# Performance work log

Measured on AMD Instinct MI355X. Metric: run time of the kernel, lower is better.

## Reference

```python
import jax, jax.numpy as jnp
import numpy as np

D = 2048      # hidden
H = 16        # heads
HD = 128      # head dim
E = 64        # experts
K = 8         # top-k
F = 1024      # expert intermediate
B, S = 1, 256
EPS = 1e-05
THETA = 10000.0
SCALE = 0.08838834764831845  # 1/sqrt(128)


def _rms(x, w):
    return x * jax.lax.rsqrt(jnp.mean(x * x, axis=-1, keepdims=True) + EPS) * w


def _rotate_half(x):
    h = x.shape[-1] // 2
    return jnp.concatenate([-x[..., h:], x[..., :h]], axis=-1)


def setup_inputs() -> dict:
    key = jax.random.key(0)
    ks = jax.random.split(key, 16)
    std = 0.02
    return {
        "x": jax.random.normal(ks[0], (B, S, D), jnp.float32),
        "ln1_w": jnp.ones((D,), jnp.float32),
        "q_w": jax.random.normal(ks[1], (D, D), jnp.float32) * std,
        "k_w": jax.random.normal(ks[2], (D, D), jnp.float32) * std,
        "v_w": jax.random.normal(ks[3], (D, D), jnp.float32) * std,
        "o_w": jax.random.normal(ks[4], (D, D), jnp.float32) * std,
        "qn_w": jnp.ones((D,), jnp.float32),
        "kn_w": jnp.ones((D,), jnp.float32),
        "ln2_w": jnp.ones((D,), jnp.float32),
        "router_w": jax.random.normal(ks[5], (E, D), jnp.float32) * std,
        "gate_w": jax.random.normal(ks[6], (E, F, D), jnp.float32) * std,
        "up_w": jax.random.normal(ks[7], (E, F, D), jnp.float32) * std,
        "down_w": jax.random.normal(ks[8], (E, D, F), jnp.float32) * std,
    }


def reference(x, ln1_w, q_w, k_w, v_w, o_w, qn_w, kn_w, ln2_w,
              router_w, gate_w, up_w, down_w):
    b, s, d = x.shape
    # ---- attention ----
    xn = _rms(x, ln1_w)
    q = _rms(jnp.einsum('bsd,od->bso', xn, q_w), qn_w)
    k = _rms(jnp.einsum('bsd,od->bso', xn, k_w), kn_w)
    v = jnp.einsum('bsd,od->bso', xn, v_w)
    q = q.reshape(b, s, H, HD).transpose(0, 2, 1, 3)  # [b,h,s,hd]
    k = k.reshape(b, s, H, HD).transpose(0, 2, 1, 3)
    v = v.reshape(b, s, H, HD).transpose(0, 2, 1, 3)
    # RoPE
    inv_freq = 1.0 / (THETA ** (jnp.arange(0, HD, 2, dtype=jnp.float32) / HD))
    ang = jnp.arange(s, dtype=jnp.float32)[:, None] * inv_freq[None, :]  # [s, hd/2]
    emb = jnp.concatenate([ang, ang], axis=-1)
    cos, sin = jnp.cos(emb).astype(x.dtype), jnp.sin(emb).astype(x.dtype)
    q = q * cos + _rotate_half(q) * sin
    k = k * cos + _rotate_half(k) * sin
    scores = jnp.einsum('bhqd,bhkd->bhqk', q, k) * SCALE
    causal = jnp.tril(jnp.ones((s, s), bool))
    scores = jnp.where(causal, scores, jnp.finfo(scores.dtype).min)
    attn = jax.nn.softmax(scores, axis=-1)
    ctx = jnp.einsum('bhqk,bhkd->bhqd', attn, v)
    ctx = ctx.transpose(0, 2, 1, 3).reshape(b, s, d)
    h = x + jnp.einsum('bsd,od->bso', ctx, o_w)
    # ---- MoE ----
    hn = _rms(h, ln2_w)
    logits = jnp.einsum('bsd,ed->bse', hn, router_w)
    probs = jax.nn.softmax(logits.astype(jnp.float32), axis=-1)
    vals, idx = jax.lax.top_k(probs, K)  # [b,s,K]
    # dense combine weights [b,s,E]; OLMoE does not renormalize top-k probs
    combine = jnp.sum(jax.nn.one_hot(idx, E, dtype=jnp.float32) * vals[..., None], axis=-2)
    combine = combine.reshape(-1, E).astype(x.dtype)  # [T,E]
    xf = hn.reshape(-1, d)                            # [T,D]
    g = jnp.einsum('td,efd->etf', xf, gate_w)         # [E,T,F]
    u = jnp.einsum('td,efd->etf', xf, up_w)
    mid = jax.nn.silu(g) * u
    eo = jnp.einsum('etf,edf->etd', mid, down_w)      # [E,T,D]
    y = jnp.einsum('te,etd->td', combine, eo).reshape(b, s, d)
    return h + y
```

## Files before the change

### kernel.cpp

```cpp
#include <hip/hip_runtime.h>
#include <math.h>

#define DHID 2048
#define TOK 256
#define NHEAD 16
#define HDIM 128
#define NEXP 64
#define KSEL 8
#define FFD 1024
#define RMSEPS 1e-5f
#define ATTNSCALE 0.08838834764831845f

typedef short bf16x8 __attribute__((ext_vector_type(8)));
typedef float f32x4 __attribute__((ext_vector_type(4)));

__device__ __forceinline__ unsigned short f2bf(float f){
  union { float f; unsigned int u; } c; c.f = f;
  unsigned int u = c.u + 0x7fffu + ((c.u>>16)&1u);
  return (unsigned short)(u>>16);
}
__device__ __forceinline__ unsigned int pk2(float a, float b){
  return (unsigned int)f2bf(a) | ((unsigned int)f2bf(b)<<16);
}
__device__ __forceinline__ bf16x8 as_bf8(uint4 u){
  union { uint4 u; bf16x8 v; } c; c.u = u; return c.v;
}

#define WAITV(N) { asm volatile("s_waitcnt vmcnt(" #N ")" ::: "memory"); __builtin_amdgcn_sched_barrier(0); }
#define WAITL0   { asm volatile("s_waitcnt lgkmcnt(0)" ::: "memory"); __builtin_amdgcn_sched_barrier(0); }
#define SB       __builtin_amdgcn_sched_barrier(0);

__global__ __launch_bounds__(256) void rms_kernel(const float* __restrict__ x,
    const float* __restrict__ w, unsigned short* __restrict__ obf,
    float* __restrict__ of32)
{
  int row = blockIdx.x, tid = threadIdx.x;
  const float* xr = x + (size_t)row*DHID;
  float4 a = *(const float4*)(xr + tid*8);
  float4 b = *(const float4*)(xr + tid*8 + 4);
  float ss = a.x*a.x+a.y*a.y+a.z*a.z+a.w*a.w + b.x*b.x+b.y*b.y+b.z*b.z+b.w*b.w;
  #pragma unroll
  for(int o=32;o>0;o>>=1) ss += __shfl_down(ss,o);
  __shared__ float red[4];
  if((tid&63)==0) red[tid>>6]=ss;
  __syncthreads();
  float r = rsqrtf((red[0]+red[1]+red[2]+red[3])*(1.0f/DHID) + RMSEPS);
  float v[8] = {a.x,a.y,a.z,a.w,b.x,b.y,b.z,b.w};
  unsigned short ob[8];
  #pragma unroll
  for(int j=0;j<8;j++){
    float val = v[j]*r*w[tid*8+j];
    ob[j]=f2bf(val);
    if(of32) of32[(size_t)row*DHID + tid*8 + j] = val;
  }
  uint4 o4;
  o4.x = (unsigned int)ob[0] | ((unsigned int)ob[1]<<16);
  o4.y = (unsigned int)ob[2] | ((unsigned int)ob[3]<<16);
  o4.z = (unsigned int)ob[4] | ((unsigned int)ob[5]<<16);
  o4.w = (unsigned int)ob[6] | ((unsigned int)ob[7]<<16);
  *(uint4*)(obf + (size_t)row*DHID + tid*8) = o4;
}

__global__ void rope_table_kernel(float* __restrict__ cs, float* __restrict__ sn){
  int i = blockIdx.x*256 + threadIdx.x;
  int s = i>>6, j = i&63;
  float invf = powf(10000.0f, -(float)j*(1.0f/64.0f));
  float ang = (float)s * invf;
  cs[i] = cosf(ang); sn[i] = sinf(ang);
}

__global__ __launch_bounds__(256) void gemm_qkv_kernel(
    const unsigned short* __restrict__ A,
    const float* __restrict__ qw, const float* __restrict__ kw, const float* __restrict__ vw,
    float* __restrict__ qo, float* __restrict__ ko, float* __restrict__ vo)
{
  int nt = blockIdx.x, mt = blockIdx.y;
  int which = nt>>5, nb = nt&31;
  const float* W = (which==0)? qw : (which==1)? kw : vw;
  float* OUT = (which==0)? qo : (which==1)? ko : vo;
  int n0 = nb*64, m0 = mt*64;
  __shared__ unsigned short As[64*64];
  __shared__ unsigned short Bs[64*64];
  int tid = threadIdx.x;
  int wid = tid>>6, lane = tid&63;
  int wm = wid>>1, wn = wid&1;
  int lr = lane&15, lg = lane>>4;
  int sr = tid>>2, sq = tid&3;
  f32x4 acc[2][2] = {};
  const unsigned short* Ap = A + (size_t)(m0+sr)*DHID + sq*16;
  const float* Bp = W + (size_t)(n0+sr)*DHID + sq*16;
  for(int k0=0;k0<DHID;k0+=64){
    uint4 a0 = *(const uint4*)(Ap + k0);
    uint4 a1 = *(const uint4*)(Ap + k0 + 8);
    float4 b0 = *(const float4*)(Bp + k0);
    float4 b1 = *(const float4*)(Bp + k0 + 4);
    float4 b2 = *(const float4*)(Bp + k0 + 8);
    float4 b3 = *(const float4*)(Bp + k0 + 12);
    int x7 = sr&7;
    *(uint4*)&As[sr*64 + (((sq*2)  ^ x7)*8)] = a0;
    *(uint4*)&As[sr*64 + (((sq*2+1)^ x7)*8)] = a1;
    uint4 p0 = make_uint4(pk2(b0.x,b0.y),pk2(b0.z,b0.w),pk2(b1.x,b1.y),pk2(b1.z,b1.w));
    uint4 p1 = make_uint4(pk2(b2.x,b2.y),pk2(b2.z,b2.w),pk2(b3.x,b3.y),pk2(b3.z,b3.w));
    *(uint4*)&Bs[sr*64 + (((sq*2)  ^ x7)*8)] = p0;
    *(uint4*)&Bs[sr*64 + (((sq*2+1)^ x7)*8)] = p1;
    __syncthreads();
    #pragma unroll
    for(int ki=0;ki<2;ki++){
      bf16x8 af[2], bfr[2];
      #pragma unroll
      for(int mi=0;mi<2;mi++){
        int r = wm*32 + mi*16 + lr;
        af[mi] = *(const bf16x8*)&As[r*64 + (((ki*4+lg)^(r&7))*8)];
      }
      #pragma unroll
      for(int ni=0;ni<2;ni++){
        int r = wn*32 + ni*16 + lr;
        bfr[ni] = *(const bf16x8*)&Bs[r*64 + (((ki*4+lg)^(r&7))*8)];
      }
      #pragma unroll
      for(int mi=0;mi<2;mi++)
        #pragma unroll
        for(int ni=0;ni<2;ni++)
          acc[mi][ni] = __builtin_amdgcn_mfma_f32_16x16x32_bf16(af[mi], bfr[ni], acc[mi][ni], 0,0,0);
    }
    __syncthreads();
  }
  #pragma unroll
  for(int mi=0;mi<2;mi++){
    #pragma unroll
    for(int ni=0;ni<2;ni++){
      int col = n0 + wn*32 + ni*16 + lr;
      int rowb = m0 + wm*32 + mi*16 + lg*4;
      #pragma unroll
      for(int rg=0;rg<4;rg++)
        OUT[(size_t)(rowb+rg)*DHID + col] = acc[mi][ni][rg];
    }
  }
}

__global__ __launch_bounds__(256) void gemm_o_kernel(const float* __restrict__ A,
  const float* __restrict__ W, const float* __restrict__ X,
  float* __restrict__ H, float* __restrict__ O)
{
  int nb = blockIdx.x, mt = blockIdx.y;
  int n0 = nb*64, m0 = mt*64;
  __shared__ unsigned short As[64*64];
  __shared__ unsigned short Bs[64*64];
  int tid = threadIdx.x;
  int wid = tid>>6, lane = tid&63;
  int wm = wid>>1, wn = wid&1;
  int lr = lane&15, lg = lane>>4;
  int sr = tid>>2, sq = tid&3;
  f32x4 acc[2][2] = {};
  const float* Ap = A + (size_t)(m0+sr)*DHID + sq*16;
  const float* Bp = W + (size_t)(n0+sr)*DHID + sq*16;
  for(int k0=0;k0<DHID;k0+=64){
    float4 a0=*(const float4*)(Ap+k0),   a1=*(const float4*)(Ap+k0+4);
    float4 a2=*(const float4*)(Ap+k0+8), a3=*(const float4*)(Ap+k0+12);
    float4 b0=*(const float4*)(Bp+k0),   b1=*(const float4*)(Bp+k0+4);
    float4 b2=*(const float4*)(Bp+k0+8), b3=*(const float4*)(Bp+k0+12);
    int x7 = sr&7;
    uint4 pa0 = make_uint4(pk2(a0.x,a0.y),pk2(a0.z,a0.w),pk2(a1.x,a1.y),pk2(a1.z,a1.w));
    uint4 pa1 = make_uint4(pk2(a2.x,a2.y),pk2(a2.z,a2.w),pk2(a3.x,a3.y),pk2(a3.z,a3.w));
    uint4 pb0 = make_uint4(pk2(b0.x,b0.y),pk2(b0.z,b0.w),pk2(b1.x,b1.y),pk2(b1.z,b1.w));
    uint4 pb1 = make_uint4(pk2(b2.x,b2.y),pk2(b2.z,b2.w),pk2(b3.x,b3.y),pk2(b3.z,b3.w));
    *(uint4*)&As[sr*64 + (((sq*2)  ^ x7)*8)] = pa0;
    *(uint4*)&As[sr*64 + (((sq*2+1)^ x7)*8)] = pa1;
    *(uint4*)&Bs[sr*64 + (((sq*2)  ^ x7)*8)] = pb0;
    *(uint4*)&Bs[sr*64 + (((sq*2+1)^ x7)*8)] = pb1;
    __syncthreads();
    #pragma unroll
    for(int ki=0;ki<2;ki++){
      bf16x8 af[2], bfr[2];
      #pragma unroll
      for(int mi=0;mi<2;mi++){
        int r = wm*32 + mi*16 + lr;
        af[mi] = *(const bf16x8*)&As[r*64 + (((ki*4+lg)^(r&7))*8)];
      }
      #pragma unroll
      for(int ni=0;ni<2;ni++){
        int r = wn*32 + ni*16 + lr;
        bfr[ni] = *(const bf16x8*)&Bs[r*64 + (((ki*4+lg)^(r&7))*8)];
      }
      #pragma unroll
      for(int mi=0;mi<2;mi++)
        #pragma unroll
        for(int ni=0;ni<2;ni++)
          acc[mi][ni] = __builtin_amdgcn_mfma_f32_16x16x32_bf16(af[mi], bfr[ni], acc[mi][ni], 0,0,0);
    }
    __syncthreads();
  }
  #pragma unroll
  for(int mi=0;mi<2;mi++){
    #pragma unroll
    for(int ni=0;ni<2;ni++){
      int col = n0 + wn*32 + ni*16 + lr;
      int rowb = m0 + wm*32 + mi*16 + lg*4;
      #pragma unroll
      for(int rg=0;rg<4;rg++){
        size_t idx = (size_t)(rowb+rg)*DHID + col;
        float v = acc[mi][ni][rg] + X[idx];
        H[idx] = v; O[idx] = v;
      }
    }
  }
}

__global__ __launch_bounds__(256) void qknorm_rope_kernel(const float* __restrict__ in,
   const float* __restrict__ w, const float* __restrict__ cs, const float* __restrict__ sn,
   float* __restrict__ out)
{
  int t = blockIdx.x, tid = threadIdx.x;
  __shared__ float xs[DHID];
  const float* xr = in + (size_t)t*DHID;
  float4 a = *(const float4*)(xr + tid*8);
  float4 b = *(const float4*)(xr + tid*8 + 4);
  *(float4*)&xs[tid*8] = a; *(float4*)&xs[tid*8+4] = b;
  float ss = a.x*a.x+a.y*a.y+a.z*a.z+a.w*a.w + b.x*b.x+b.y*b.y+b.z*b.z+b.w*b.w;
  #pragma unroll
  for(int o=32;o>0;o>>=1) ss += __shfl_down(ss,o);
  __shared__ float red[4];
  if((tid&63)==0) red[tid>>6]=ss;
  __syncthreads();
  float r = rsqrtf((red[0]+red[1]+red[2]+red[3])*(1.0f/DHID) + RMSEPS);
  int hh = tid>>4, jb = (tid&15)*4;
  #pragma unroll
  for(int p=0;p<4;p++){
    int j = jb+p;
    int i0 = hh*HDIM + j, i1 = i0+64;
    float va = xs[i0]*r*w[i0];
    float vb = xs[i1]*r*w[i1];
    float c = cs[t*64+j], s = sn[t*64+j];
    out[((size_t)(hh*TOK + t))*HDIM + j]    = va*c - vb*s;
    out[((size_t)(hh*TOK + t))*HDIM + j+64] = vb*c + va*s;
  }
}

__global__ __launch_bounds__(256) void attn_kernel(const float* __restrict__ qh,
  const float* __restrict__ kh, const float* __restrict__ vf, float* __restrict__ ctx)
{
  int head = blockIdx.x>>4, qt = blockIdx.x&15;
  __shared__ float qs[16][132];
  __shared__ float sc[16][260];
  __shared__ float red[16][16];
  __shared__ float rmx[16], rsm[16];
  int tid = threadIdx.x;
  {
    int r = tid>>4, c = (tid&15)*8;
    const float* src = qh + ((size_t)(head*TOK + qt*16 + r))*HDIM + c;
    *(float4*)&qs[r][c]   = *(const float4*)(src);
    *(float4*)&qs[r][c+4] = *(const float4*)(src+4);
  }
  __syncthreads();
  int qi = tid&15, kk = tid>>4;
  int qg = qt*16 + qi;
  for(int k=kk; k<=qg; k+=16){
    const float* kp = kh + ((size_t)(head*TOK + k))*HDIM;
    float d = 0.f;
    #pragma unroll 8
    for(int c=0;c<128;c+=4){
      float4 kv = *(const float4*)(kp + c);
      float4 qv = *(const float4*)&qs[qi][c];
      d += qv.x*kv.x + qv.y*kv.y + qv.z*kv.z + qv.w*kv.w;
    }
    sc[qi][k] = d*ATTNSCALE;
  }
  float m = -1e30f;
  for(int k=kk;k<=qg;k+=16) m = fmaxf(m, sc[qi][k]);
  red[qi][kk] = m;
  __syncthreads();
  if(kk==0){
    float mm=-1e30f;
    #pragma unroll
    for(int j=0;j<16;j++) mm = fmaxf(mm, red[qi][j]);
    rmx[qi]=mm;
  }
  __syncthreads();
  float mm = rmx[qi];
  float s = 0.f;
  for(int k=kk;k<=qg;k+=16){ float pp = expf(sc[qi][k]-mm); sc[qi][k]=pp; s+=pp; }
  red[qi][kk]=s;
  __syncthreads();
  if(kk==0){
    float t_=0.f;
    #pragma unroll
    for(int j=0;j<16;j++) t_ += red[qi][j];
    rsm[qi]=t_;
  }
  __syncthreads();
  int dg = kk;
  float acc[8]={0,0,0,0,0,0,0,0};
  const float* vp = vf + head*HDIM + dg*8;
  for(int k=0;k<=qg;k++){
    float p = sc[qi][k];
    float4 v0 = *(const float4*)(vp + (size_t)k*DHID);
    float4 v1 = *(const float4*)(vp + (size_t)k*DHID + 4);
    acc[0]+=p*v0.x; acc[1]+=p*v0.y; acc[2]+=p*v0.z; acc[3]+=p*v0.w;
    acc[4]+=p*v1.x; acc[5]+=p*v1.y; acc[6]+=p*v1.z; acc[7]+=p*v1.w;
  }
  float inv = 1.0f/rsm[qi];
  float* op = ctx + ((size_t)(qt*16+qi))*DHID + head*HDIM + dg*8;
  *(float4*)(op)   = make_float4(acc[0]*inv, acc[1]*inv, acc[2]*inv, acc[3]*inv);
  *(float4*)(op+4) = make_float4(acc[4]*inv, acc[5]*inv, acc[6]*inv, acc[7]*inv);
}

__global__ __launch_bounds__(256) void router_kernel(const float* __restrict__ hn,
    const float* __restrict__ rw, int* __restrict__ counts, int* __restrict__ toklist,
    float* __restrict__ wlist)
{
  int t = blockIdx.x, tid = threadIdx.x;
  __shared__ float xs[DHID];
  __shared__ float part[NEXP*4];
  __shared__ float probs[NEXP];
  *(float4*)&xs[tid*8]   = *(const float4*)(hn + (size_t)t*DHID + tid*8);
  *(float4*)&xs[tid*8+4] = *(const float4*)(hn + (size_t)t*DHID + tid*8+4);
  __syncthreads();
  int e = tid&63, c = tid>>6;
  const float* w = rw + (size_t)e*DHID + c*512;
  const float* xc = xs + c*512;
  float d = 0.f;
  for(int i=0;i<512;i+=4){
    float4 wv = *(const float4*)(w+i);
    d += xc[i]*wv.x + xc[i+1]*wv.y + xc[i+2]*wv.z + xc[i+3]*wv.w;
  }
  part[c*64 + e] = d;
  __syncthreads();
  if(tid<64){
    float logit = part[tid] + part[64+tid] + part[128+tid] + part[192+tid];
    float m = logit;
    #pragma unroll
    for(int o=32;o>0;o>>=1) m = fmaxf(m, __shfl_xor(m,o));
    float p = expf(logit - m);
    float s = p;
    #pragma unroll
    for(int o=32;o>0;o>>=1) s += __shfl_xor(s,o);
    probs[tid] = p/s;
  }
  __syncthreads();
  if(tid==0){
    unsigned long long used = 0ull;
    for(int r=0;r<KSEL;r++){
      float best = -1.f; int bi = 0;
      for(int j=0;j<NEXP;j++){
        if(!((used>>j)&1ull) && probs[j]>best){ best=probs[j]; bi=j; }
      }
      used |= (1ull<<bi);
      int slot = atomicAdd(&counts[bi],1);
      toklist[bi*TOK+slot] = t;
      wlist[bi*TOK+slot] = best;
    }
  }
}

__global__ void scan_kernel(const int* __restrict__ counts, int* __restrict__ offs){
  int e = threadIdx.x;
  int c = counts[e];
  int v = c;
  #pragma unroll
  for(int o=1;o<64;o<<=1){
    int n = __shfl_up(v,o);
    if(e>=o) v += n;
  }
  offs[e] = v - c;
}

__global__ __launch_bounds__(256,2) void moe_gateup_kernel(const unsigned short* __restrict__ hnb,
  const float* __restrict__ gw, const float* __restrict__ uw,
  const int* __restrict__ counts, const int* __restrict__ offs,
  const int* __restrict__ toklist, const float* __restrict__ wlist,
  unsigned short* __restrict__ mid)
{
  int fb = blockIdx.x, e = blockIdx.y, mc = blockIdx.z;
  int cnt = counts[e];
  if(mc*32 >= cnt) return;
  int base = offs[e];
  __shared__ unsigned short Gs[64*256];
  __shared__ unsigned short Us[64*256];
  int tid = threadIdx.x, w = tid>>6, lane = tid&63;
  int wm = w>>1, wn = w&1, lr = lane&15, lg = lane>>4;
  int srow = tid>>2, sc4 = tid&3, rx = srow&7;
  int halfo = (sc4&1)*4, vbase = sc4>>1;

  const float* Gp = gw + ((size_t)e*FFD + fb*64 + srow)*DHID + sc4*4;
  const float* Up = uw + ((size_t)e*FFD + fb*64 + srow)*DHID + sc4*4;
  int aslot = mc*32 + wm*16 + lr;
  int acl = (aslot<cnt)? aslot : (cnt-1);
  const unsigned short* Ap = hnb + (size_t)toklist[e*TOK+acl]*DHID + lg*8;

  f32x4 ag[2]={}, au[2]={};
  float4 P[8], Q[8];
  uint4 av[8];

  #define ISSUE(BK,SRC,s,jb) { \
    _Pragma("unroll") \
    for(int j=0;j<8;j++) BK[j] = *(const float4*)(SRC + (s)*256 + ((jb)+j)*16); }
  #define WRITE(BK,DST,jb) { \
    _Pragma("unroll") \
    for(int j=0;j<8;j++){ \
      int v = ((jb)+j)*2 + vbase; \
      int vp = (v & ~7) | ((v&7) ^ rx); \
      uint2 val; val.x = pk2(BK[j].x,BK[j].y); val.y = pk2(BK[j].z,BK[j].w); \
      *(uint2*)&DST[srow*256 + vp*8 + halfo] = val; } }
  #define ISSUE_A(s) { \
    _Pragma("unroll") \
    for(int kf=0;kf<8;kf++) av[kf] = *(const uint4*)(Ap + (s)*256 + kf*32); }
  #define COMPUTE() { \
    _Pragma("unroll") \
    for(int kf=0;kf<8;kf++){ \
      bf16x8 af = as_bf8(av[kf]); \
      _Pragma("unroll") \
      for(int ni=0;ni<2;ni++){ \
        int R = wn*32 + ni*16 + lr; \
        int v = kf*4 + lg; \
        int vp = (v & ~7) | ((v&7) ^ (lr&7)); \
        int ho = R*256 + vp*8; \
        bf16x8 gfr = *(const bf16x8*)&Gs[ho]; \
        bf16x8 ufr = *(const bf16x8*)&Us[ho]; \
        ag[ni] = __builtin_amdgcn_mfma_f32_16x16x32_bf16(af, gfr, ag[ni], 0,0,0); \
        au[ni] = __builtin_amdgcn_mfma_f32_16x16x32_bf16(af, ufr, au[ni], 0,0,0); \
      } \
    } }

  const int NS = DHID/256;
  ISSUE(P, Gp, 0, 0)
  ISSUE(Q, Gp, 0, 8)
  for(int s=0;s<NS;s++){
    WAITV(8)
    WRITE(P, Gs, 0)
    ISSUE(P, Up, s, 0)
    WAITV(8)
    WRITE(Q, Gs, 8)
    ISSUE(Q, Up, s, 8)
    WAITV(8)
    WRITE(P, Us, 0)
    ISSUE_A(s)
    WAITV(8)
    WRITE(Q, Us, 8)
    if(s+1<NS){ ISSUE(P, Gp, s+1, 0) }
    WAITL0
    __builtin_amdgcn_s_barrier(); SB
    if(s+1<NS){ WAITV(8) } else { WAITV(0) }
    COMPUTE()
    if(s+1<NS){ ISSUE(Q, Gp, s+1, 8) }
    __builtin_amdgcn_s_barrier(); SB
  }
  #undef ISSUE
  #undef WRITE
  #undef ISSUE_A
  #undef COMPUTE

  #pragma unroll
  for(int ni=0;ni<2;ni++){
    int f = fb*64 + wn*32 + ni*16 + lr;
    #pragma unroll
    for(int rg=0;rg<4;rg++){
      int sl = wm*16 + lg*4 + rg;
      int slot = mc*32 + sl;
      if(slot < cnt){
        float cw = wlist[e*TOK + slot];
        float g = ag[ni][rg], u = au[ni][rg];
        float mval = g/(1.0f+expf(-g))*u*cw;
        mid[((size_t)(base+slot))*FFD + f] = f2bf(mval);
      }
    }
  }
}

__global__ __launch_bounds__(256,3) void moe_down_kernel(const unsigned short* __restrict__ mid,
  const float* __restrict__ dwn, const int* __restrict__ counts, const int* __restrict__ offs,
  const int* __restrict__ toklist, float* __restrict__ out)
{
  int nb=blockIdx.x, e=blockIdx.y, mc=blockIdx.z;
  int cnt=counts[e];
  if(mc*32>=cnt) return;
  int base=offs[e];
  __shared__ unsigned short Ds[64*256];
  int tid=threadIdx.x, w=tid>>6, lane=tid&63;
  int wm=w>>1, wn=w&1, lr=lane&15, lg=lane>>4;
  int srow=tid>>2, sc4=tid&3, rx=srow&7;
  int halfo=(sc4&1)*4, vbase=sc4>>1;

  const float* Dp = dwn + ((size_t)e*DHID + nb*64 + srow)*FFD + sc4*4;
  int slot0 = mc*32 + wm*16 + lr;
  int sla = (slot0<cnt)? slot0 : (cnt-1);
  const unsigned short* Ap = mid + (size_t)(base+sla)*FFD + lg*8;

  f32x4 acc[2]={};
  float4 P[8], Q[8];
  uint4 av[8];

  #define ISSUE(BK,s,jb) { \
    _Pragma("unroll") \
    for(int j=0;j<8;j++) BK[j] = *(const float4*)(Dp + (s)*256 + ((jb)+j)*16); }
  #define WRITE(BK,jb) { \
    _Pragma("unroll") \
    for(int j=0;j<8;j++){ \
      int v = ((jb)+j)*2 + vbase; \
      int vp = (v & ~7) | ((v&7) ^ rx); \
      uint2 val; val.x = pk2(BK[j].x,BK[j].y); val.y = pk2(BK[j].z,BK[j].w); \
      *(uint2*)&Ds[srow*256 + vp*8 + halfo] = val; } }
  #define ISSUE_A(s) { \
    _Pragma("unroll") \
    for(int kf=0;kf<8;kf++) av[kf] = *(const uint4*)(Ap + (s)*256 + kf*32); }
  #define COMPUTE() { \
    _Pragma("unroll") \
    for(int kf=0;kf<8;kf++){ \
      bf16x8 af = as_bf8(av[kf]); \
      _Pragma("unroll") \
      for(int ni=0;ni<2;ni++){ \
        int R = wn*32 + ni*16 + lr; \
        int v = kf*4 + lg; \
        int vp = (v & ~7) | ((v&7) ^ (lr&7)); \
        bf16x8 dfr = *(const bf16x8*)&Ds[R*256 + vp*8]; \
        acc[ni] = __builtin_amdgcn_mfma_f32_16x16x32_bf16(af, dfr, acc[ni], 0,0,0); \
      } \
    } }

  const int NS = FFD/256;
  ISSUE(P, 0, 0)
  ISSUE(Q, 0, 8)
  for(int s=0;s<NS;s++){
    WAITV(8)
    WRITE(P, 0)
    ISSUE_A(s)
    WAITV(8)
    WRITE(Q, 8)
    if(s+1<NS){ ISSUE(P, s+1, 0) }
    WAITL0
    __builtin_amdgcn_s_barrier(); SB
    if(s+1<NS){ WAITV(8) } else { WAITV(0) }
    COMPUTE()
    if(s+1<NS){ ISSUE(Q, s+1, 8) }
    __builtin_amdgcn_s_barrier(); SB
  }
  #undef ISSUE
  #undef WRITE
  #undef ISSUE_A
  #undef COMPUTE

  #pragma unroll
  for(int ni=0;ni<2;ni++){
    int d = nb*64 + wn*32 + ni*16 + lr;
    #pragma unroll
    for(int rg=0;rg<4;rg++){
      int sl=wm*16+lg*4+rg, slot=mc*32+sl;
      if(slot<cnt){
        int tok = toklist[e*TOK + slot];
        atomicAdd(out + (size_t)tok*DHID + d, acc[ni][rg]);
      }
    }
  }
}

extern "C" void kernel_launch(void* const* d_in, const int* in_sizes, int n_in,
                              void* d_out, int out_size, void* d_ws, size_t ws_size,
                              hipStream_t stream)
{
  (void)in_sizes; (void)n_in; (void)out_size; (void)ws_size;
  const float* x    = (const float*)d_in[0];
  const float* ln1w = (const float*)d_in[1];
  const float* qw   = (const float*)d_in[2];
  const float* kw   = (const float*)d_in[3];
  const float* vw   = (const float*)d_in[4];
  const float* ow   = (const float*)d_in[5];
  const float* qnw  = (const float*)d_in[6];
  const float* knw  = (const float*)d_in[7];
  const float* ln2w = (const float*)d_in[8];
  const float* rw   = (const float*)d_in[9];
  const float* gw   = (const float*)d_in[10];
  const float* uw   = (const float*)d_in[11];
  const float* dwn  = (const float*)d_in[12];
  float* out = (float*)d_out;

  char* p = (char*)d_ws;
  auto alloc = [&](size_t bytes)->void*{ void* r = (void*)p; p += (bytes + 255) & ~(size_t)255; return r; };
  unsigned short* xnb = (unsigned short*)alloc((size_t)TOK*DHID*2);
  float* qf   = (float*)alloc((size_t)TOK*DHID*4);
  float* kf   = (float*)alloc((size_t)TOK*DHID*4);
  float* vf   = (float*)alloc((size_t)TOK*DHID*4);
  float* qh   = (float*)alloc((size_t)TOK*DHID*4);
  float* kh   = (float*)alloc((size_t)TOK*DHID*4);
  float* ctx  = (float*)alloc((size_t)TOK*DHID*4);
  float* hbuf = (float*)alloc((size_t)TOK*DHID*4);
  float* hnf  = (float*)alloc((size_t)TOK*DHID*4);
  unsigned short* hnb = (unsigned short*)alloc((size_t)TOK*DHID*2);
  float* csb  = (float*)alloc((size_t)TOK*64*4);
  float* snb  = (float*)alloc((size_t)TOK*64*4);
  int* counts = (int*)alloc(NEXP*4);
  int* offs   = (int*)alloc(NEXP*4);
  int* toklist= (int*)alloc((size_t)NEXP*TOK*4);
  float* wlist= (float*)alloc((size_t)NEXP*TOK*4);
  unsigned short* mid = (unsigned short*)alloc((size_t)TOK*KSEL*FFD*2);

  rope_table_kernel<<<64,256,0,stream>>>(csb,snb);
  rms_kernel<<<TOK,256,0,stream>>>(x, ln1w, xnb, nullptr);
  gemm_qkv_kernel<<<dim3(96,4),256,0,stream>>>(xnb,qw,kw,vw,qf,kf,vf);
  qknorm_rope_kernel<<<TOK,256,0,stream>>>(qf,qnw,csb,snb,qh);
  qknorm_rope_kernel<<<TOK,256,0,stream>>>(kf,knw,csb,snb,kh);
  attn_kernel<<<256,256,0,stream>>>(qh,kh,vf,ctx);
  gemm_o_kernel<<<dim3(32,4),256,0,stream>>>(ctx,ow,x,hbuf,out);
  rms_kernel<<<TOK,256,0,stream>>>(hbuf, ln2w, hnb, hnf);
  hipMemsetAsync(counts,0,NEXP*4,stream);
  router_kernel<<<TOK,256,0,stream>>>(hnf,rw,counts,toklist,wlist);
  scan_kernel<<<1,64,0,stream>>>(counts,offs);
  moe_gateup_kernel<<<dim3(16,NEXP,8),256,0,stream>>>(hnb,gw,uw,counts,offs,toklist,wlist,mid);
  moe_down_kernel<<<dim3(32,NEXP,8),256,0,stream>>>(mid,dwn,counts,offs,toklist,out);
}
```

Before: 642.2 us.

## Drop rope-table and scan launches, compute inline; use nontemporal weight loads

The RoPE cos/sin table kernel is removed and the angles are computed inline with powf/cosf/sinf in the qk-norm kernel. The expert-offset scan kernel is removed; each MoE block recomputes the prefix sum over counts with wave shuffles and shares it through LDS after a barrier. Expert weight loads in the gate/up and down kernels now use nontemporal loads so the streamed fp32 weights are less likely to pollute the cache. This saves two kernel launches but adds redundant transcendental and scan work per block, plus an extra __syncthreads.

New measurement: 691.9 us. +7.7%, slower.

```diff
diff --git a/kernel.cpp b/kernel.cpp
--- a/kernel.cpp
+++ b/kernel.cpp
@@ -13,6 +13,8 @@
 
 typedef short bf16x8 __attribute__((ext_vector_type(8)));
 typedef float f32x4 __attribute__((ext_vector_type(4)));
+typedef float f4 __attribute__((ext_vector_type(4)));
+typedef unsigned int u4 __attribute__((ext_vector_type(4)));
 
 __device__ __forceinline__ unsigned short f2bf(float f){
   union { float f; unsigned int u; } c; c.f = f;
@@ -59,14 +61,6 @@
   o4.z = (unsigned int)ob[4] | ((unsigned int)ob[5]<<16);
   o4.w = (unsigned int)ob[6] | ((unsigned int)ob[7]<<16);
   *(uint4*)(obf + (size_t)row*DHID + tid*8) = o4;
-}
-
-__global__ void rope_table_kernel(float* __restrict__ cs, float* __restrict__ sn){
-  int i = blockIdx.x*256 + threadIdx.x;
-  int s = i>>6, j = i&63;
-  float invf = powf(10000.0f, -(float)j*(1.0f/64.0f));
-  float ang = (float)s * invf;
-  cs[i] = cosf(ang); sn[i] = sinf(ang);
 }
 
 __global__ __launch_bounds__(256) void gemm_qkv_kernel(
@@ -207,8 +201,7 @@
 }
 
 __global__ __launch_bounds__(256) void qknorm_rope_kernel(const float* __restrict__ in,
-   const float* __restrict__ w, const float* __restrict__ cs, const float* __restrict__ sn,
-   float* __restrict__ out)
+   const float* __restrict__ w, float* __restrict__ out)
 {
   int t = blockIdx.x, tid = threadIdx.x;
   __shared__ float xs[DHID];
@@ -230,7 +223,9 @@
     int i0 = hh*HDIM + j, i1 = i0+64;
     float va = xs[i0]*r*w[i0];
     float vb = xs[i1]*r*w[i1];
-    float c = cs[t*64+j], s = sn[t*64+j];
+    float invf = powf(10000.0f, -(float)j*(1.0f/64.0f));
+    float ang = (float)t * invf;
+    float c = cosf(ang), s = sinf(ang);
     out[((size_t)(hh*TOK + t))*HDIM + j]    = va*c - vb*s;
     out[((size_t)(hh*TOK + t))*HDIM + j+64] = vb*c + va*s;
   }
@@ -352,31 +347,27 @@
   }
 }
 
-__global__ void scan_kernel(const int* __restrict__ counts, int* __restrict__ offs){
-  int e = threadIdx.x;
-  int c = counts[e];
-  int v = c;
-  #pragma unroll
-  for(int o=1;o<64;o<<=1){
-    int n = __shfl_up(v,o);
-    if(e>=o) v += n;
-  }
-  offs[e] = v - c;
-}
-
 __global__ __launch_bounds__(256,2) void moe_gateup_kernel(const unsigned short* __restrict__ hnb,
   const float* __restrict__ gw, const float* __restrict__ uw,
-  const int* __restrict__ counts, const int* __restrict__ offs,
+  const int* __restrict__ counts,
   const int* __restrict__ toklist, const float* __restrict__ wlist,
   unsigned short* __restrict__ mid)
 {
   int fb = blockIdx.x, e = blockIdx.y, mc = blockIdx.z;
   int cnt = counts[e];
   if(mc*32 >= cnt) return;
-  int base = offs[e];
+  int tid = threadIdx.x;
+  __shared__ int sbase;
+  if(tid<64){
+    int c = counts[tid];
+    int v = c;
+    #pragma unroll
+    for(int o=1;o<64;o<<=1){ int n=__shfl_up(v,o); if(tid>=o) v+=n; }
+    if(tid==e) sbase = v - c;
+  }
   __shared__ unsigned short Gs[64*256];
   __shared__ unsigned short Us[64*256];
-  int tid = threadIdx.x, w = tid>>6, lane = tid&63;
+  int w = tid>>6, lane = tid&63;
   int wm = w>>1, wn = w&1, lr = lane&15, lg = lane>>4;
   int srow = tid>>2, sc4 = tid&3, rx = srow&7;
   int halfo = (sc4&1)*4, vbase = sc4>>1;
@@ -386,20 +377,22 @@
   int aslot = mc*32 + wm*16 + lr;
   int acl = (aslot<cnt)? aslot : (cnt-1);
   const unsigned short* Ap = hnb + (size_t)toklist[e*TOK+acl]*DHID + lg*8;
+  __syncthreads();
+  int base = sbase;
 
   f32x4 ag[2]={}, au[2]={};
-  float4 P[8], Q[8];
+  f4 P[8], Q[8];
   uint4 av[8];
 
   #define ISSUE(BK,SRC,s,jb) { \
     _Pragma("unroll") \
-    for(int j=0;j<8;j++) BK[j] = *(const float4*)(SRC + (s)*256 + ((jb)+j)*16); }
+    for(int j=0;j<8;j++) BK[j] = __builtin_nontemporal_load((const f4*)(SRC + (s)*256 + ((jb)+j)*16)); }
   #define WRITE(BK,DST,jb) { \
     _Pragma("unroll") \
     for(int j=0;j<8;j++){ \
       int v = ((jb)+j)*2 + vbase; \
       int vp = (v & ~7) | ((v&7) ^ rx); \
-      uint2 val; val.x = pk2(BK[j].x,BK[j].y); val.y = pk2(BK[j].z,BK[j].w); \
+      uint2 val; val.x = pk2(BK[j][0],BK[j][1]); val.y = pk2(BK[j][2],BK[j][3]); \
       *(uint2*)&DST[srow*256 + vp*8 + halfo] = val; } }
   #define ISSUE_A(s) { \
     _Pragma("unroll") \
@@ -467,37 +460,47 @@
 }
 
 __global__ __launch_bounds__(256,3) void moe_down_kernel(const unsigned short* __restrict__ mid,
-  const float* __restrict__ dwn, const int* __restrict__ counts, const int* __restrict__ offs,
+  const float* __restrict__ dwn, const int* __restrict__ counts,
   const int* __restrict__ toklist, float* __restrict__ out)
 {
   int nb=blockIdx.x, e=blockIdx.y, mc=blockIdx.z;
   int cnt=counts[e];
   if(mc*32>=cnt) return;
-  int base=offs[e];
+  int tid=threadIdx.x;
+  __shared__ int sbase;
+  if(tid<64){
+    int c = counts[tid];
+    int v = c;
+    #pragma unroll
+    for(int o=1;o<64;o<<=1){ int n=__shfl_up(v,o); if(tid>=o) v+=n; }
+    if(tid==e) sbase = v - c;
+  }
   __shared__ unsigned short Ds[64*256];
-  int tid=threadIdx.x, w=tid>>6, lane=tid&63;
+  int w=tid>>6, lane=tid&63;
   int wm=w>>1, wn=w&1, lr=lane&15, lg=lane>>4;
   int srow=tid>>2, sc4=tid&3, rx=srow&7;
   int halfo=(sc4&1)*4, vbase=sc4>>1;
 
   const float* Dp = dwn + ((size_t)e*DHID + nb*64 + srow)*FFD + sc4*4;
+  __syncthreads();
+  int base = sbase;
   int slot0 = mc*32 + wm*16 + lr;
   int sla = (slot0<cnt)? slot0 : (cnt-1);
   const unsigned short* Ap = mid + (size_t)(base+sla)*FFD + lg*8;
 
   f32x4 acc[2]={};
-  float4 P[8], Q[8];
+  f4 P[8], Q[8];
   uint4 av[8];
 
   #define ISSUE(BK,s,jb) { \
     _Pragma("unroll") \
-    for(int j=0;j<8;j++) BK[j] = *(const float4*)(Dp + (s)*256 + ((jb)+j)*16); }
+    for(int j=0;j<8;j++) BK[j] = __builtin_nontemporal_load((const f4*)(Dp + (s)*256 + ((jb)+j)*16)); }
   #define WRITE(BK,jb) { \
     _Pragma("unroll") \
     for(int j=0;j<8;j++){ \
       int v = ((jb)+j)*2 + vbase; \
       int vp = (v & ~7) | ((v&7) ^ rx); \
-      uint2 val; val.x = pk2(BK[j].x,BK[j].y); val.y = pk2(BK[j].z,BK[j].w); \
+      uint2 val; val.x = pk2(BK[j][0],BK[j][1]); val.y = pk2(BK[j][2],BK[j][3]); \
       *(uint2*)&Ds[srow*256 + vp*8 + halfo] = val; } }
   #define ISSUE_A(s) { \
     _Pragma("unroll") \
@@ -584,25 +587,20 @@
   float* hbuf = (float*)alloc((size_t)TOK*DHID*4);
   float* hnf  = (float*)alloc((size_t)TOK*DHID*4);
   unsigned short* hnb = (unsigned short*)alloc((size_t)TOK*DHID*2);
-  float* csb  = (float*)alloc((size_t)TOK*64*4);
-  float* snb  = (float*)alloc((size_t)TOK*64*4);
   int* counts = (int*)alloc(NEXP*4);
-  int* offs   = (int*)alloc(NEXP*4);
   int* toklist= (int*)alloc((size_t)NEXP*TOK*4);
   float* wlist= (float*)alloc((size_t)NEXP*TOK*4);
   unsigned short* mid = (unsigned short*)alloc((size_t)TOK*KSEL*FFD*2);
 
-  rope_table_kernel<<<64,256,0,stream>>>(csb,snb);
   rms_kernel<<<TOK,256,0,stream>>>(x, ln1w, xnb, nullptr);
   gemm_qkv_kernel<<<dim3(96,4),256,0,stream>>>(xnb,qw,kw,vw,qf,kf,vf);
-  qknorm_rope_kernel<<<TOK,256,0,stream>>>(qf,qnw,csb,snb,qh);
-  qknorm_rope_kernel<<<TOK,256,0,stream>>>(kf,knw,csb,snb,kh);
+  qknorm_rope_kernel<<<TOK,256,0,stream>>>(qf,qnw,qh);
+  qknorm_rope_kernel<<<TOK,256,0,stream>>>(kf,knw,kh);
   attn_kernel<<<256,256,0,stream>>>(qh,kh,vf,ctx);
   gemm_o_kernel<<<dim3(32,4),256,0,stream>>>(ctx,ow,x,hbuf,out);
   rms_kernel<<<TOK,256,0,stream>>>(hbuf, ln2w, hnb, hnf);
   hipMemsetAsync(counts,0,NEXP*4,stream);
   router_kernel<<<TOK,256,0,stream>>>(hnf,rw,counts,toklist,wlist);
-  scan_kernel<<<1,64,0,stream>>>(counts,offs);
-  moe_gateup_kernel<<<dim3(16,NEXP,8),256,0,stream>>>(hnb,gw,uw,counts,offs,toklist,wlist,mid);
-  moe_down_kernel<<<dim3(32,NEXP,8),256,0,stream>>>(mid,dwn,counts,offs,toklist,out);
-}
+  moe_gateup_kernel<<<dim3(16,NEXP,8),256,0,stream>>>(hnb,gw,uw,counts,toklist,wlist,mid);
+  moe_down_kernel<<<dim3(32,NEXP,8),256,0,stream>>>(mid,dwn,counts,toklist,out);
+}
```
